# Performance work log

Measured on AMD Instinct MI355X. Metric: run time of the kernel, lower is better.

## Reference

```python
import jax, jax.numpy as jnp
import numpy as np

B, T, P, U = 2, 50, 5111, 64


def setup_inputs() -> dict:
    key = jax.random.key(0)
    ks = jax.random.split(key, 12)
    data_target = jax.random.randint(ks[0], (B, T), 0, P)
    data_cor = jax.random.randint(ks[1], (B, T), 0, 2)
    # X: bi-LSTM max-pooled problem encodings [P, 2U]
    X = jax.random.normal(ks[2], (P, 2 * U), dtype=jnp.float32) * 0.1
    # cos_X: cosine similarity of X with itself (as in call_encode)
    norm = jnp.sqrt(jnp.sum(X * X, axis=1))
    cos_X = (X @ X.T) / (norm[:, None] * norm[None, :])
    # causal lower-triangular aggregation mask [T, T]
    trimatrix = jnp.tril(jnp.ones((T, T), dtype=jnp.float32))
    # frozen embedding2 table [2, 4U]
    emb2 = jax.random.uniform(ks[3], (2, 4 * U), minval=-1.0, maxval=1.0, dtype=jnp.float32)
    # LSTM params (keras gate order i,f,c,o), input dim 4U
    s = 0.1549193338
    Wk = jax.random.uniform(ks[4], (4 * U, 4 * U), minval=-s, maxval=s, dtype=jnp.float32)
    Wr = jax.random.normal(ks[5], (U, 4 * U), dtype=jnp.float32) * 0.05  # orthogonal-ish stand-in
    bl = jnp.concatenate([jnp.zeros((U,)), jnp.ones((U,)), jnp.zeros((2 * U,))]).astype(jnp.float32)  # unit forget bias
    s1 = 0.1732050808
    W1 = jax.random.uniform(ks[6], (3 * U, 50), minval=-s1, maxval=s1, dtype=jnp.float32)
    b1 = jnp.zeros((50,), dtype=jnp.float32)
    s2 = 0.3429971703
    W2 = jax.random.uniform(ks[7], (50, 1), minval=-s2, maxval=s2, dtype=jnp.float32)
    b2 = jnp.zeros((1,), dtype=jnp.float32)
    return {"data_target": data_target, "data_cor": data_cor, "num_pro": P,
            "X": X, "cos_X": cos_X, "trimatrix": trimatrix, "emb2": emb2,
            "Wk": Wk, "Wr": Wr, "bl": bl, "W1": W1, "b1": b1, "W2": W2, "b2": b2}


def _lstm(x, Wk, Wr, bl):
    # x: [B, T, D] -> h: [B, T, U]; keras LSTM math, gate order i,f,g,o
    u = Wr.shape[0]
    xT = jnp.swapaxes(x, 0, 1)  # [T, B, D]
    h0 = jnp.zeros((x.shape[0], u), x.dtype)
    c0 = jnp.zeros((x.shape[0], u), x.dtype)

    def step(carry, xt):
        h, c = carry
        z = xt @ Wk + h @ Wr + bl
        i, f, g, o = jnp.split(z, 4, axis=-1)
        c = jax.nn.sigmoid(f) * c + jax.nn.sigmoid(i) * jnp.tanh(g)
        h = jax.nn.sigmoid(o) * jnp.tanh(c)
        return (h, c), h

    _, hs = jax.lax.scan(step, (h0, c0), xT)
    return jnp.swapaxes(hs, 0, 1)


def reference(data_target, data_cor, num_pro, X, cos_X, trimatrix, emb2, Wk, Wr, bl, W1, b1, W2, b2):
    # one_hot @ X == gather
    t_X = X[data_target]                             # [B,T,2U]
    t_X = jnp.concatenate([t_X, t_X], axis=-1)       # [B,T,4U]
    xt = t_X * emb2[data_cor]                        # [B,T,4U]
    ht = _lstm(xt, Wk, Wr, bl)                       # [B,T,U]
    # attention aggregation: a[b,t,p] = cos_X[target[b,t], p]
    a = cos_X[data_target]                           # [B,T,P]
    # ajhj[b,s,p,u] = sum_t trimatrix[t,s] * a[b,t,p] * ht[b,t,u]
    ajhj = jnp.einsum('btp,btu,ts->bspu', a, ht, trimatrix)  # [B,T,P,U]
    XX = jnp.broadcast_to(X[None, None], (ajhj.shape[0], ajhj.shape[1], num_pro, X.shape[1]))
    hatt = jnp.concatenate([ajhj, XX], axis=-1)      # [B,T,P,3U]
    r = jax.nn.relu(hatt @ W1 + b1)                  # [B,T,P,50]
    r = r @ W2 + b2                                  # [B,T,P,1]
    return r
```

## Files before the change

kernel.cpp:

```cpp
#include <hip/hip_runtime.h>
#include <math.h>

#define B_ 2
#define T_ 50
#define P_ 5111
#define U_ 64

__global__ __launch_bounds__(256) void pre_kernel(
    const int* __restrict__ tgt, const int* __restrict__ cor,
    const float* __restrict__ X, const float* __restrict__ emb2,
    const float* __restrict__ Wk, const float* __restrict__ W1,
    const float* __restrict__ b1,
    float* __restrict__ ZX, float* __restrict__ XWT) {
  __shared__ float xe[256];
  __shared__ float xrow[4][128];
  const int blk = blockIdx.x;
  const int tid = threadIdx.x;
  if (blk < B_ * T_) {
    const int t_ = tgt[blk], c_ = cor[blk];
    xe[tid] = X[t_ * 128 + (tid & 127)] * emb2[c_ * 256 + tid];
    __syncthreads();
    float z = 0.f;
#pragma unroll 8
    for (int d = 0; d < 256; ++d)
      z = fmaf(xe[d], Wk[d * 256 + tid], z);
    ZX[blk * 256 + tid] = z;
  } else {
    const int sub = tid >> 6, lane = tid & 63;
    const int p = (blk - B_ * T_) * 4 + sub;
    if (p < P_) {
      xrow[sub][lane]      = X[p * 128 + lane];
      xrow[sub][64 + lane] = X[p * 128 + 64 + lane];
    }
    __syncthreads();
    if (p < P_ && lane < 50) {
      float acc = b1[lane];
#pragma unroll 16
      for (int u = 0; u < 128; ++u)
        acc = fmaf(xrow[sub][u], W1[(64 + u) * 50 + lane], acc);
      XWT[lane * P_ + p] = acc;
    }
  }
}

__global__ __launch_bounds__(320) void lstm_kernel(
    const float* __restrict__ ZX, const float* __restrict__ Wr,
    const float* __restrict__ bl, const float* __restrict__ W1,
    float* __restrict__ G) {
  const int b = blockIdx.x;
  const int k = threadIdx.x;
  __shared__ __align__(16) float h_s[2][64];
  __shared__ float G_s[T_][50];
  const bool is_z = (k < 256);
  const bool is_g = (k >= 256) && (k < 306);
  const int g   = k & 3;
  const int u   = k >> 2;
  const int col = g * 64 + u;
  const int j   = k - 256;

  float w[64];
  float blv = 0.f, znext = 0.f;
  if (is_z) {
#pragma unroll
    for (int u2 = 0; u2 < 64; ++u2) w[u2] = Wr[u2 * 256 + col];
    blv = bl[col];
    znext = ZX[(b * T_) * 256 + col];
  } else if (is_g) {
#pragma unroll
    for (int u2 = 0; u2 < 64; ++u2) w[u2] = W1[u2 * 50 + j];
  }
  if (k < 64) h_s[0][k] = 0.f;
  float c = 0.f;
  __syncthreads();

  for (int t = 0; t < T_; ++t) {
    const int rb = t & 1, wb = rb ^ 1;
    const float zcur = znext;
    if (is_z && t + 1 < T_) znext = ZX[(b * T_ + t + 1) * 256 + col];
    float a0 = 0.f, a1 = 0.f, a2 = 0.f, a3 = 0.f;
    if (is_z || is_g) {
      const float4* h4 = (const float4*)h_s[rb];
#pragma unroll
      for (int q = 0; q < 16; ++q) {
        const float4 hq = h4[q];
        a0 = fmaf(hq.x, w[4 * q + 0], a0);
        a1 = fmaf(hq.y, w[4 * q + 1], a1);
        a2 = fmaf(hq.z, w[4 * q + 2], a2);
        a3 = fmaf(hq.w, w[4 * q + 3], a3);
      }
    }
    const float mv = (a0 + a1) + (a2 + a3);
    if (is_z) {
      const float z = mv + zcur + blv;
      const bool isg2 = (g == 2);
      const float arg = isg2 ? (2.f * z) : (-z);
      const float e   = __expf(arg);
      const float v   = __fdividef(1.f, 1.f + e);
      const float res = isg2 ? fmaf(-2.f, v, 1.f) : v;
      const float v1 = __shfl_xor(res, 1);
      const float v2 = __shfl_xor(res, 2);
      const float v3 = __shfl_xor(res, 3);
      const float ig = (g == 0) ? res : (g == 1) ? v1 : (g == 2) ? v2 : v3;
      const float fg = (g == 1) ? res : (g == 0) ? v1 : (g == 3) ? v2 : v3;
      const float gg = (g == 2) ? res : (g == 3) ? v1 : (g == 0) ? v2 : v3;
      const float og = (g == 3) ? res : (g == 2) ? v1 : (g == 1) ? v2 : v3;
      c = fmaf(fg, c, ig * gg);
      const float e2 = __expf(2.f * c);
      const float th = fmaf(-2.f, __fdividef(1.f, 1.f + e2), 1.f);
      if (g == 0) h_s[wb][u] = og * th;
    } else if (is_g && t > 0) {
      G_s[t - 1][j] = mv;
    }
    __syncthreads();
  }
  if (is_g) {
    const float4* h4 = (const float4*)h_s[T_ & 1];
    float a0 = 0.f, a1 = 0.f, a2 = 0.f, a3 = 0.f;
#pragma unroll
    for (int q = 0; q < 16; ++q) {
      const float4 hq = h4[q];
      a0 = fmaf(hq.x, w[4 * q + 0], a0);
      a1 = fmaf(hq.y, w[4 * q + 1], a1);
      a2 = fmaf(hq.z, w[4 * q + 2], a2);
      a3 = fmaf(hq.w, w[4 * q + 3], a3);
    }
    G_s[T_ - 1][j] = (a0 + a1) + (a2 + a3);
  }
  __syncthreads();
  for (int i = k; i < T_ * 50; i += 320)
    G[b * T_ * 50 + i] = (&G_s[0][0])[i];
}

__global__ __launch_bounds__(256) void out_kernel(
    const int* __restrict__ tgt, const float* __restrict__ cosX,
    const float* __restrict__ G, const float* __restrict__ XWT,
    const float* __restrict__ W2, const float* __restrict__ b2,
    float* __restrict__ out) {
  const int b   = blockIdx.y;
  const int tid = threadIdx.x;
  const int p   = blockIdx.x * 256 + tid;
  __shared__ float G_s[T_ * 50];
  __shared__ float W2_s[50];
  __shared__ int   tgt_s[T_];
  for (int i = tid; i < T_ * 50; i += 256) G_s[i] = G[b * T_ * 50 + i];
  if (tid < 50) {
    W2_s[tid]  = W2[tid];
    tgt_s[tid] = tgt[b * T_ + tid];
  }
  __syncthreads();
  if (p >= P_) return;
  float S[50];
#pragma unroll
  for (int j = 0; j < 50; ++j) S[j] = XWT[j * P_ + p];
  const float b2v = b2[0];
  float av = cosX[tgt_s[T_ - 1] * P_ + p];
  for (int s = T_ - 1; s >= 0; --s) {
    const float av_next = (s > 0) ? cosX[tgt_s[s - 1] * P_ + p] : 0.f;
    const float* Gs = &G_s[s * 50];
    float acc = b2v;
#pragma unroll
    for (int j = 0; j < 50; ++j) {
      S[j] = fmaf(av, Gs[j], S[j]);
      acc  = fmaf(fmaxf(S[j], 0.f), W2_s[j], acc);
    }
    out[(b * T_ + s) * P_ + p] = acc;
    av = av_next;
  }
}

extern "C" void kernel_launch(void* const* d_in, const int* in_sizes, int n_in,
                              void* d_out, int out_size, void* d_ws, size_t ws_size,
                              hipStream_t stream) {
  const int*   tgt  = (const int*)d_in[0];
  const int*   cor  = (const int*)d_in[1];
  const float* X    = (const float*)d_in[3];
  const float* cosX = (const float*)d_in[4];
  const float* emb2 = (const float*)d_in[6];
  const float* Wk   = (const float*)d_in[7];
  const float* Wr   = (const float*)d_in[8];
  const float* bl   = (const float*)d_in[9];
  const float* W1   = (const float*)d_in[10];
  const float* b1   = (const float*)d_in[11];
  const float* W2   = (const float*)d_in[12];
  const float* b2   = (const float*)d_in[13];
  float* out = (float*)d_out;

  float* ws  = (float*)d_ws;
  float* ZX  = ws;
  float* G   = ws + 25600;
  float* XWT = ws + 30600;

  const int xw_blocks = (P_ + 3) / 4;
  pre_kernel<<<dim3(B_ * T_ + xw_blocks), dim3(256), 0, stream>>>(
      tgt, cor, X, emb2, Wk, W1, b1, ZX, XWT);
  lstm_kernel<<<dim3(B_), dim3(320), 0, stream>>>(ZX, Wr, bl, W1, G);
  out_kernel<<<dim3((P_ + 255) / 256, B_), dim3(256), 0, stream>>>(
      tgt, cosX, G, XWT, W2, b2, out);
}
```

Before: 251.3 us.

## Fuse XWT projection into LSTM launch, defer G projection, pack FMAs as v2f

The XWT projection moves out of the pre-kernel and into the same launch as the LSTM blocks, so the serial LSTM recurrence overlaps with the independent XW work. The LSTM now keeps every hidden state in shared memory and computes the G projection after the loop as a parallel v2f pass, instead of using dedicated threads in each step. Inner loops in the LSTM and output kernels use packed 2-wide FMA vectors, and shuffles become DPP quad permutes. The risks are extra shared memory per block and the LSTM blocks possibly being scheduled after many XWT blocks.

```diff
diff --git a/kernel.cpp b/kernel.cpp
--- a/kernel.cpp
+++ b/kernel.cpp
@@ -6,28 +6,40 @@
 #define P_ 5111
 #define U_ 64
 
-__global__ __launch_bounds__(256) void pre_kernel(
+typedef float v2f __attribute__((ext_vector_type(2)));
+
+#define QPERM(x, ctrl)                                                        \
+  __int_as_float(__builtin_amdgcn_mov_dpp(__float_as_int(x), (ctrl), 0xf, 0xf, true))
+
+__global__ __launch_bounds__(256) void zx_kernel(
     const int* __restrict__ tgt, const int* __restrict__ cor,
     const float* __restrict__ X, const float* __restrict__ emb2,
-    const float* __restrict__ Wk, const float* __restrict__ W1,
-    const float* __restrict__ b1,
-    float* __restrict__ ZX, float* __restrict__ XWT) {
+    const float* __restrict__ Wk, float* __restrict__ ZX) {
+  const int bt = blockIdx.x;
+  const int k  = threadIdx.x;
   __shared__ float xe[256];
-  __shared__ float xrow[4][128];
+  const int t_ = tgt[bt], c_ = cor[bt];
+  xe[k] = X[t_ * 128 + (k & 127)] * emb2[c_ * 256 + k];
+  __syncthreads();
+  float z = 0.f;
+#pragma unroll 8
+  for (int d = 0; d < 256; ++d)
+    z = fmaf(xe[d], Wk[d * 256 + k], z);
+  ZX[bt * 256 + k] = z;
+}
+
+__global__ __launch_bounds__(256) void lstm_xwt_kernel(
+    const float* __restrict__ ZX, const float* __restrict__ Wr,
+    const float* __restrict__ bl, const float* __restrict__ W1,
+    const float* __restrict__ X, const float* __restrict__ b1,
+    float* __restrict__ G, float* __restrict__ XWT) {
   const int blk = blockIdx.x;
-  const int tid = threadIdx.x;
-  if (blk < B_ * T_) {
-    const int t_ = tgt[blk], c_ = cor[blk];
-    xe[tid] = X[t_ * 128 + (tid & 127)] * emb2[c_ * 256 + tid];
-    __syncthreads();
-    float z = 0.f;
-#pragma unroll 8
-    for (int d = 0; d < 256; ++d)
-      z = fmaf(xe[d], Wk[d * 256 + tid], z);
-    ZX[blk * 256 + tid] = z;
-  } else {
-    const int sub = tid >> 6, lane = tid & 63;
-    const int p = (blk - B_ * T_) * 4 + sub;
+  const int k   = threadIdx.x;
+
+  if (blk >= B_) {
+    __shared__ float xrow[4][128];
+    const int sub = k >> 6, lane = k & 63;
+    const int p = (blk - B_) * 4 + sub;
     if (p < P_) {
       xrow[sub][lane]      = X[p * 128 + lane];
       xrow[sub][64 + lane] = X[p * 128 + 64 + lane];
@@ -40,95 +52,81 @@
         acc = fmaf(xrow[sub][u], W1[(64 + u) * 50 + lane], acc);
       XWT[lane * P_ + p] = acc;
     }
-  }
-}
-
-__global__ __launch_bounds__(320) void lstm_kernel(
-    const float* __restrict__ ZX, const float* __restrict__ Wr,
-    const float* __restrict__ bl, const float* __restrict__ W1,
-    float* __restrict__ G) {
-  const int b = blockIdx.x;
-  const int k = threadIdx.x;
-  __shared__ __align__(16) float h_s[2][64];
-  __shared__ float G_s[T_][50];
-  const bool is_z = (k < 256);
-  const bool is_g = (k >= 256) && (k < 306);
+    return;
+  }
+
+  const int b   = blk;
   const int g   = k & 3;
   const int u   = k >> 2;
   const int col = g * 64 + u;
-  const int j   = k - 256;
-
-  float w[64];
-  float blv = 0.f, znext = 0.f;
-  if (is_z) {
-#pragma unroll
-    for (int u2 = 0; u2 < 64; ++u2) w[u2] = Wr[u2 * 256 + col];
-    blv = bl[col];
-    znext = ZX[(b * T_) * 256 + col];
-  } else if (is_g) {
-#pragma unroll
-    for (int u2 = 0; u2 < 64; ++u2) w[u2] = W1[u2 * 50 + j];
-  }
-  if (k < 64) h_s[0][k] = 0.f;
+  __shared__ __align__(16) float H_s[T_ + 1][64];
+  __shared__ __align__(16) float W1_s[64 * 50];
+
+  v2f w2[32];
+#pragma unroll
+  for (int i = 0; i < 32; ++i) {
+    v2f t; t.x = Wr[(2 * i) * 256 + col]; t.y = Wr[(2 * i + 1) * 256 + col];
+    w2[i] = t;
+  }
+  const float blv = bl[col];
+  float znext = ZX[(b * T_) * 256 + col];
+  for (int i = k; i < 64 * 50; i += 256) W1_s[i] = W1[i];
+  if (k < 64) H_s[0][k] = 0.f;
   float c = 0.f;
   __syncthreads();
 
   for (int t = 0; t < T_; ++t) {
-    const int rb = t & 1, wb = rb ^ 1;
     const float zcur = znext;
-    if (is_z && t + 1 < T_) znext = ZX[(b * T_ + t + 1) * 256 + col];
-    float a0 = 0.f, a1 = 0.f, a2 = 0.f, a3 = 0.f;
-    if (is_z || is_g) {
-      const float4* h4 = (const float4*)h_s[rb];
-#pragma unroll
-      for (int q = 0; q < 16; ++q) {
-        const float4 hq = h4[q];
-        a0 = fmaf(hq.x, w[4 * q + 0], a0);
-        a1 = fmaf(hq.y, w[4 * q + 1], a1);
-        a2 = fmaf(hq.z, w[4 * q + 2], a2);
-        a3 = fmaf(hq.w, w[4 * q + 3], a3);
-      }
-    }
-    const float mv = (a0 + a1) + (a2 + a3);
-    if (is_z) {
-      const float z = mv + zcur + blv;
-      const bool isg2 = (g == 2);
-      const float arg = isg2 ? (2.f * z) : (-z);
-      const float e   = __expf(arg);
-      const float v   = __fdividef(1.f, 1.f + e);
-      const float res = isg2 ? fmaf(-2.f, v, 1.f) : v;
-      const float v1 = __shfl_xor(res, 1);
-      const float v2 = __shfl_xor(res, 2);
-      const float v3 = __shfl_xor(res, 3);
-      const float ig = (g == 0) ? res : (g == 1) ? v1 : (g == 2) ? v2 : v3;
-      const float fg = (g == 1) ? res : (g == 0) ? v1 : (g == 3) ? v2 : v3;
-      const float gg = (g == 2) ? res : (g == 3) ? v1 : (g == 0) ? v2 : v3;
-      const float og = (g == 3) ? res : (g == 2) ? v1 : (g == 1) ? v2 : v3;
-      c = fmaf(fg, c, ig * gg);
-      const float e2 = __expf(2.f * c);
-      const float th = fmaf(-2.f, __fdividef(1.f, 1.f + e2), 1.f);
-      if (g == 0) h_s[wb][u] = og * th;
-    } else if (is_g && t > 0) {
-      G_s[t - 1][j] = mv;
-    }
-    __syncthreads();
-  }
-  if (is_g) {
-    const float4* h4 = (const float4*)h_s[T_ & 1];
-    float a0 = 0.f, a1 = 0.f, a2 = 0.f, a3 = 0.f;
+    if (t + 1 < T_) znext = ZX[(b * T_ + t + 1) * 256 + col];
+    const float4* h4 = (const float4*)&H_s[t][0];
+    v2f a0 = {0.f, 0.f}, a1 = {0.f, 0.f}, a2 = {0.f, 0.f}, a3 = {0.f, 0.f};
 #pragma unroll
     for (int q = 0; q < 16; ++q) {
       const float4 hq = h4[q];
-      a0 = fmaf(hq.x, w[4 * q + 0], a0);
-      a1 = fmaf(hq.y, w[4 * q + 1], a1);
-      a2 = fmaf(hq.z, w[4 * q + 2], a2);
-      a3 = fmaf(hq.w, w[4 * q + 3], a3);
-    }
-    G_s[T_ - 1][j] = (a0 + a1) + (a2 + a3);
-  }
-  __syncthreads();
-  for (int i = k; i < T_ * 50; i += 320)
-    G[b * T_ * 50 + i] = (&G_s[0][0])[i];
+      v2f hlo; hlo.x = hq.x; hlo.y = hq.y;
+      v2f hhi; hhi.x = hq.z; hhi.y = hq.w;
+      if (q & 1) {
+        a2 = __builtin_elementwise_fma(hlo, w2[2 * q], a2);
+        a3 = __builtin_elementwise_fma(hhi, w2[2 * q + 1], a3);
+      } else {
+        a0 = __builtin_elementwise_fma(hlo, w2[2 * q], a0);
+        a1 = __builtin_elementwise_fma(hhi, w2[2 * q + 1], a1);
+      }
+    }
+    const v2f as = (a0 + a2) + (a1 + a3);
+    const float z = as.x + as.y + zcur + blv;
+    const bool isg2 = (g == 2);
+    const float arg = isg2 ? (2.f * z) : (-z);
+    const float e   = __expf(arg);
+    const float v   = __fdividef(1.f, 1.f + e);
+    const float res = isg2 ? fmaf(-2.f, v, 1.f) : v;
+    const float v1 = QPERM(res, 177);
+    const float v2 = QPERM(res, 78);
+    const float v3 = QPERM(res, 27);
+    const float ig = (g == 0) ? res : (g == 1) ? v1 : (g == 2) ? v2 : v3;
+    const float fg = (g == 1) ? res : (g == 0) ? v1 : (g == 3) ? v2 : v3;
+    const float gg = (g == 2) ? res : (g == 3) ? v1 : (g == 0) ? v2 : v3;
+    const float og = (g == 3) ? res : (g == 2) ? v1 : (g == 1) ? v2 : v3;
+    c = fmaf(fg, c, ig * gg);
+    const float th = fmaf(-2.f, __fdividef(1.f, 1.f + __expf(2.f * c)), 1.f);
+    if (g == 0) H_s[t + 1][u] = og * th;
+    __syncthreads();
+  }
+
+  const v2f* W1_2 = (const v2f*)W1_s;
+  v2f*       G_2  = (v2f*)G;
+  for (int task = k; task < T_ * 25; task += 256) {
+    const int t  = task / 25;
+    const int jp = task % 25;
+    const float* hrow = &H_s[t + 1][0];
+    v2f acc = {0.f, 0.f};
+#pragma unroll
+    for (int u2 = 0; u2 < 64; ++u2) {
+      v2f hb; hb.x = hrow[u2]; hb.y = hrow[u2];
+      acc = __builtin_elementwise_fma(hb, W1_2[u2 * 25 + jp], acc);
+    }
+    G_2[b * (T_ * 25) + task] = acc;
+  }
 }
 
 __global__ __launch_bounds__(256) void out_kernel(
@@ -139,9 +137,9 @@
   const int b   = blockIdx.y;
   const int tid = threadIdx.x;
   const int p   = blockIdx.x * 256 + tid;
-  __shared__ float G_s[T_ * 50];
-  __shared__ float W2_s[50];
-  __shared__ int   tgt_s[T_];
+  __shared__ __align__(16) float G_s[T_ * 50];
+  __shared__ __align__(16) float W2_s[50];
+  __shared__ int tgt_s[T_];
   for (int i = tid; i < T_ * 50; i += 256) G_s[i] = G[b * T_ * 50 + i];
   if (tid < 50) {
     W2_s[tid]  = W2[tid];
@@ -149,21 +147,28 @@
   }
   __syncthreads();
   if (p >= P_) return;
-  float S[50];
-#pragma unroll
-  for (int j = 0; j < 50; ++j) S[j] = XWT[j * P_ + p];
+  v2f S2[25];
+#pragma unroll
+  for (int jj = 0; jj < 25; ++jj) {
+    v2f t; t.x = XWT[(2 * jj) * P_ + p]; t.y = XWT[(2 * jj + 1) * P_ + p];
+    S2[jj] = t;
+  }
+  const v2f* W2_2 = (const v2f*)W2_s;
   const float b2v = b2[0];
+  const v2f zero2 = {0.f, 0.f};
   float av = cosX[tgt_s[T_ - 1] * P_ + p];
   for (int s = T_ - 1; s >= 0; --s) {
     const float av_next = (s > 0) ? cosX[tgt_s[s - 1] * P_ + p] : 0.f;
-    const float* Gs = &G_s[s * 50];
-    float acc = b2v;
-#pragma unroll
-    for (int j = 0; j < 50; ++j) {
-      S[j] = fmaf(av, Gs[j], S[j]);
-      acc  = fmaf(fmaxf(S[j], 0.f), W2_s[j], acc);
-    }
-    out[(b * T_ + s) * P_ + p] = acc;
+    const v2f* G2 = (const v2f*)&G_s[s * 50];
+    v2f av2; av2.x = av; av2.y = av;
+    v2f acc2; acc2.x = b2v; acc2.y = 0.f;
+#pragma unroll
+    for (int jj = 0; jj < 25; ++jj) {
+      S2[jj] = __builtin_elementwise_fma(av2, G2[jj], S2[jj]);
+      const v2f r = __builtin_elementwise_max(S2[jj], zero2);
+      acc2 = __builtin_elementwise_fma(r, W2_2[jj], acc2);
+    }
+    out[(b * T_ + s) * P_ + p] = acc2.x + acc2.y;
     av = av_next;
   }
 }
@@ -191,9 +196,9 @@
   float* XWT = ws + 30600;
 
   const int xw_blocks = (P_ + 3) / 4;
-  pre_kernel<<<dim3(B_ * T_ + xw_blocks), dim3(256), 0, stream>>>(
-      tgt, cor, X, emb2, Wk, W1, b1, ZX, XWT);
-  lstm_kernel<<<dim3(B_), dim3(320), 0, stream>>>(ZX, Wr, bl, W1, G);
+  zx_kernel<<<dim3(B_ * T_), dim3(256), 0, stream>>>(tgt, cor, X, emb2, Wk, ZX);
+  lstm_xwt_kernel<<<dim3(B_ + xw_blocks), dim3(256), 0, stream>>>(
+      ZX, Wr, bl, W1, X, b1, G, XWT);
   out_kernel<<<dim3((P_ + 255) / 256, B_), dim3(256), 0, stream>>>(
       tgt, cosX, G, XWT, W2, b2, out);
 }
```

Measured after the change: 250.7 us. About the same (-0.2%).
